# Optimization experiments

Hardware: AMD Instinct MI355X
Metric: run time of the kernel (lower is better)

The kernel has to match this reference:

```python
import jax, jax.numpy as jnp
import numpy as np

EMB = 768
HEADS = 12
DH = EMB // HEADS


def setup_inputs() -> dict:
    key = jax.random.key(0)
    k = jax.random.split(key, 5)
    s = 0.02
    return {
        "x": jax.random.normal(k[0], (4, 2048, EMB), dtype=jnp.float32),
        "qkv_w": jax.random.normal(k[1], (3 * EMB, EMB), dtype=jnp.float32) * s,  # torch Linear weight [out,in]
        "qkv_b": jax.random.normal(k[2], (3 * EMB,), dtype=jnp.float32) * s,
        "proj_w": jax.random.normal(k[3], (EMB, EMB), dtype=jnp.float32) * s,
        "proj_b": jax.random.normal(k[4], (EMB,), dtype=jnp.float32) * s,
    }


def reference(x, qkv_w, qkv_b, proj_w, proj_b):
    b, n, _ = x.shape
    qkv = x @ qkv_w.T + qkv_b  # [b, n, 3*EMB]
    # rearrange 'b n (h d qkv) -> qkv b h n d'
    qkv = qkv.reshape(b, n, HEADS, DH, 3)
    qkv = jnp.transpose(qkv, (4, 0, 2, 1, 3))  # [3, b, h, n, d]
    q, k, v = qkv[0], qkv[1], qkv[2]
    e = jnp.einsum("bhqd,bhkd->bhqk", q, k)
    scale = jnp.float32(EMB) ** 0.5
    # NOTE: original divides by sqrt(emb_size) AFTER softmax (faithful to source)
    attn = jax.nn.softmax(e, axis=-1) / scale
    out = jnp.einsum("bhqk,bhkd->bhqd", attn, v)
    out = jnp.transpose(out, (0, 2, 1, 3)).reshape(b, n, EMB)  # 'b h n d -> b n (h d)'
    return out @ proj_w.T + proj_b
```

## Files before the change

### kernel.cpp

```cpp
#include <hip/hip_runtime.h>
#include <hip/hip_bf16.h>

typedef unsigned short ushort_t;
typedef __attribute__((ext_vector_type(8))) short s16x8;
typedef __attribute__((ext_vector_type(4))) float f32x4;
typedef __attribute__((ext_vector_type(16))) float f32x16;
typedef __attribute__((ext_vector_type(4))) unsigned int u32x4;

#define EMB 768
#define HEADS 12
#define DH 64
#define BATCH 4
#define SEQ 2048
#define MTOK (BATCH*SEQ)
#define NQKV (3*EMB)
#define LOG2E 1.44269504088896f

__device__ __forceinline__ ushort_t f2bf(float f) {
  unsigned u = __float_as_uint(f);
  u += 0x7fffu + ((u >> 16) & 1u);
  return (ushort_t)(u >> 16);
}
__device__ __forceinline__ unsigned pk2bf(float a, float b) {
  return (unsigned)f2bf(a) | ((unsigned)f2bf(b) << 16);
}
__device__ __forceinline__ unsigned cvtpk(float lo, float hi_) {
  unsigned d;
  asm("v_cvt_pk_bf16_f32 %0, %1, %2" : "=v"(d) : "v"(lo), "v"(hi_));
  return d;
}

__device__ __forceinline__ void gload_lds16(const void* g, void* l) {
  __builtin_amdgcn_global_load_lds(
      (const __attribute__((address_space(1))) unsigned*)g,
      (__attribute__((address_space(3))) unsigned*)l, 16, 0, 0);
}

__global__ void cvt_bf16(const float* __restrict__ in, ushort_t* __restrict__ out, int n4) {
  int i = blockIdx.x * blockDim.x + threadIdx.x;
  if (i >= n4) return;
  const float4 v = reinterpret_cast<const float4*>(in)[i];
  reinterpret_cast<uint2*>(out)[i] = make_uint2(pk2bf(v.x, v.y), pk2bf(v.z, v.w));
}

__global__ void cvt_wqkv(const float* __restrict__ w, const float* __restrict__ bias,
                         ushort_t* __restrict__ out, float* __restrict__ bias_p, int n4) {
  int i = blockIdx.x * blockDim.x + threadIdx.x;
  if (i >= n4) return;
  const int srcrow = i / 192;
  const int c4 = i - srcrow * 192;
  const int h = srcrow / 192;
  const int rem = srcrow - h * 192;
  const int d = rem / 3;
  const int which = rem - d * 3;
  const int dstrow = which * 768 + h * 64 + d;
  const float4 v = reinterpret_cast<const float4*>(w)[i];
  reinterpret_cast<uint2*>(out)[dstrow * 192 + c4] =
      make_uint2(pk2bf(v.x, v.y), pk2bf(v.z, v.w));
  if (c4 == 0) bias_p[dstrow] = bias[srcrow];
}

#define TM 128
#define TN 128
#define NSTEP 24

template<int MODE>
__global__ __launch_bounds__(256, 3) void gemm_bt(
    const ushort_t* __restrict__ A, const ushort_t* __restrict__ BT,
    const float* __restrict__ bias, float* __restrict__ Cf,
    ushort_t* __restrict__ Qd, ushort_t* __restrict__ Kd, ushort_t* __restrict__ Vt,
    int M, int N, int K)
{
  __shared__ alignas(16) ushort_t As[3][TM*32];
  __shared__ alignas(16) ushort_t Bs[3][TN*32];
  const int t = threadIdx.x;
  const int w = t >> 6, l = t & 63, g = l >> 4, r = l & 15;
  const int wr = w >> 1, wc = w & 1;
  int lin = blockIdx.y * gridDim.x + blockIdx.x;
  const int cpx = (gridDim.x * gridDim.y) >> 3;
  lin = (lin & 7) * cpx + (lin >> 3);
  const int m0 = (lin / gridDim.x) * TM, n0 = (lin - (lin / gridDim.x) * gridDim.x) * TN;

  f32x4 acc[4][4] = {};

#define GSTAGE(bufc, st)                                                           \
  {                                                                                \
    const int kt = (st) * 32;                                                      \
    _Pragma("unroll")                                                              \
    for (int p = 0; p < 2; ++p) {                                                  \
      const int i = t + p * 256;                              \
      const int row = i >> 2, c8 = (i & 3) * 8;                                    \
      gload_lds16(A  + (size_t)(m0 + row) * K + kt + c8,                           \
                  (char*)&As[bufc][0] + i * 16);                                   \
      gload_lds16(BT + (size_t)(n0 + row) * K + kt + c8,                           \
                  (char*)&Bs[bufc][0] + i * 16);                                   \
    }                                                                              \
  }

#define GCOMP(bufc)                                                                \
  {                                                                                \
    const char* ab = (const char*)&As[bufc][0] + wr * 4096 + r * 64 + g * 16;      \
    const char* bb = (const char*)&Bs[bufc][0] + wc * 4096 + r * 64 + g * 16;      \
    s16x8 fa[4], fb[4];                                                            \
    _Pragma("unroll")                                                              \
    for (int mi = 0; mi < 4; ++mi) {                                               \
      fa[mi] = *(const s16x8*)(ab + mi * 1024);                                    \
      fb[mi] = *(const s16x8*)(bb + mi * 1024);                                    \
    }                                                                              \
    __builtin_amdgcn_s_setprio(1);                                                 \
    _Pragma("unroll")                                                              \
    for (int mi = 0; mi < 4; ++mi)                                                 \
      _Pragma("unroll")                                                            \
      for (int ni = 0; ni < 4; ++ni)                                               \
        acc[mi][ni] = __builtin_amdgcn_mfma_f32_16x16x32_bf16(                     \
            fa[mi], fb[ni], acc[mi][ni], 0, 0, 0);                                 \
    __builtin_amdgcn_s_setprio(0);                                                 \
  }

#define GITER(bufcur, bufn2, st)                                                   \
  {                                                                                \
    asm volatile("s_barrier" ::: "memory");                                        \
    { const int s2 = (st) + 2 < NSTEP ? (st) + 2 : NSTEP - 1; GSTAGE(bufn2, s2); } \
    asm volatile("s_waitcnt vmcnt(8)" ::: "memory");                               \
    asm volatile("s_barrier" ::: "memory");                                        \
    GCOMP(bufcur);                                                                 \
  }

  GSTAGE(0, 0);
  GSTAGE(1, 1);
  for (int s = 0; s < NSTEP - 3; s += 3) {
    GITER(0, 2, s);
    GITER(1, 0, s + 1);
    GITER(2, 1, s + 2);
  }
  GITER(0, 2, 21);
  GITER(1, 0, 22);
  GITER(2, 1, 23);
#undef GITER
#undef GCOMP
#undef GSTAGE

#pragma unroll
  for (int ni = 0; ni < 4; ++ni) {
    const int col = n0 + wc*64 + ni*16 + r;
    const float bv = bias[col];
    if (MODE == 0) {
#pragma unroll
      for (int mi = 0; mi < 4; ++mi)
#pragma unroll
        for (int q = 0; q < 4; ++q) {
          const int rowg = m0 + wr*64 + mi*16 + g*4 + q;
          Cf[(size_t)rowg * N + col] = acc[mi][ni][q] + bv;
        }
    } else {
      const int which = col / 768;
      const int h_ = (col - which * 768) >> 6;
      const int d_ = col & 63;
      if (which == 2) {
#pragma unroll
        for (int mi = 0; mi < 4; ++mi) {
          const int nn0 = m0 + wr*64 + mi*16 + g*4;
          const int bb = nn0 >> 11, nl = nn0 & 2047;
          const int np0 = (nl & ~12) | ((nl & 4) << 1) | ((nl & 8) >> 1);
          uint2 u;
          u.x = pk2bf(acc[mi][ni][0] + bv, acc[mi][ni][1] + bv);
          u.y = pk2bf(acc[mi][ni][2] + bv, acc[mi][ni][3] + bv);
          *reinterpret_cast<uint2*>(Vt + ((size_t)(bb*HEADS + h_)*DH + d_)*SEQ + np0) = u;
        }
      } else {
        ushort_t* dst = (which == 0) ? Qd : Kd;
        const float sc = (which == 0) ? LOG2E : 1.0f;
#pragma unroll
        for (int mi = 0; mi < 4; ++mi)
#pragma unroll
          for (int q = 0; q < 4; ++q) {
            const int rowg = m0 + wr*64 + mi*16 + g*4 + q;
            const int bb = rowg >> 11, nn = rowg & 2047;
            dst[((size_t)(bb*HEADS + h_)*SEQ + nn)*DH + d_] =
                f2bf((acc[mi][ni][q] + bv) * sc);
          }
      }
    }
  }
}

#define NTIL 32

__global__ __launch_bounds__(256, 3) void attn_fwd(
    const ushort_t* __restrict__ Qd, const ushort_t* __restrict__ Kd,
    const ushort_t* __restrict__ Vt, ushort_t* __restrict__ Oa)
{
  __shared__ alignas(16) char L[3][16384];
  char* Lc = &L[0][0];

  const int t = threadIdx.x;
  const int w = t >> 6, l = t & 63;
  const int c31 = l & 31, hi = l >> 5;
  const int blk = blockIdx.x;
  const int logical = (blk & 7) * 96 + (blk >> 3);
  const int bh = logical >> 4;
  const int qt = logical & 15;
  const int q0 = qt * 128 + w * 32;
  const int b = bh / HEADS, h = bh - b * HEADS;

  const ushort_t* Qp = Qd + (size_t)bh * SEQ * DH;
  const ushort_t* Kp = Kd + (size_t)bh * SEQ * DH;
  const ushort_t* Vp = Vt + (size_t)bh * DH * SEQ;

  s16x8 qf[4];
  {
    const ushort_t* qp = Qp + (size_t)(q0 + c31) * DH + hi * 8;
#pragma unroll
    for (int c = 0; c < 4; ++c) qf[c] = *(const s16x8*)(qp + c * 16);
  }

  f32x16 oacc0 = {}, oacc1 = {};
  float ps0 = 0.f, ps1 = 0.f, ps2 = 0.f, ps3 = 0.f;

  const int ldsb = hi * 1024 + c31 * 16;
  const ushort_t* ksrc0 = Kp + (size_t)l * DH + w * 16;
  const ushort_t* vsrc0 = Vp + (size_t)l * SEQ + w * 16;
  char* kdst0 = Lc + w * 2048 + l * 16;

#define STAGE(bufc, tile_)                                                         \
  {                                                                                \
    const int tl = (tile_);                                                        \
    const ushort_t* ks = ksrc0 + (size_t)tl * (64 * DH);                           \
    const ushort_t* vs = vsrc0 + tl * 64;                                          \
    char* kd = kdst0 + (bufc) * 16384;                                             \
    gload_lds16(ks,     kd);                                                       \
    gload_lds16(ks + 8, kd + 1024);                                                \
    gload_lds16(vs,     kd + 8192);                                                \
    gload_lds16(vs + 8, kd + 9216);                                                \
  }

#define KGROUP(bufc, kg)                                                           \
  {                                                                                \
    const char* base = Lc + (bufc) * 16384 + ldsb;                                 \
    s16x8 kf0 = *(const s16x8*)(base + ((kg)*512 + 0*2048));                       \
    s16x8 kf1 = *(const s16x8*)(base + ((kg)*512 + 1*2048));                       \
    s16x8 kf2 = *(const s16x8*)(base + ((kg)*512 + 2*2048));                       \
    s16x8 kf3 = *(const s16x8*)(base + ((kg)*512 + 3*2048));                       \
    s16x8 va00 = *(const s16x8*)(base + (8192 + (kg)*4096 + 0*2048 + 0*512));      \
    s16x8 va01 = *(const s16x8*)(base + (8192 + (kg)*4096 + 1*2048 + 0*512));      \
    s16x8 va10 = *(const s16x8*)(base + (8192 + (kg)*4096 + 0*2048 + 1*512));      \
    s16x8 va11 = *(const s16x8*)(base + (8192 + (kg)*4096 + 1*2048 + 1*512));      \
    __builtin_amdgcn_s_setprio(1);                                                 \
    f32x16 s = {};                                                                 \
    s = __builtin_amdgcn_mfma_f32_32x32x16_bf16(kf0, qf[0], s, 0, 0, 0);           \
    s = __builtin_amdgcn_mfma_f32_32x32x16_bf16(kf1, qf[1], s, 0, 0, 0);           \
    s = __builtin_amdgcn_mfma_f32_32x32x16_bf16(kf2, qf[2], s, 0, 0, 0);           \
    s = __builtin_amdgcn_mfma_f32_32x32x16_bf16(kf3, qf[3], s, 0, 0, 0);           \
    __builtin_amdgcn_s_setprio(0);                                                 \
    float pe[16];                                                                  \
    _Pragma("unroll")                                                              \
    for (int r2 = 0; r2 < 16; ++r2) pe[r2] = __builtin_amdgcn_exp2f(s[r2]);        \
    ps0 += (pe[0]  + pe[1])  + (pe[2]  + pe[3]);                                   \
    ps1 += (pe[4]  + pe[5])  + (pe[6]  + pe[7]);                                   \
    ps2 += (pe[8]  + pe[9])  + (pe[10] + pe[11]);                                  \
    ps3 += (pe[12] + pe[13]) + (pe[14] + pe[15]);                                  \
    u32x4 f0u = { cvtpk(pe[0],  pe[1]),  cvtpk(pe[2],  pe[3]),                     \
                  cvtpk(pe[4],  pe[5]),  cvtpk(pe[6],  pe[7]) };                   \
    u32x4 f1u = { cvtpk(pe[8],  pe[9]),  cvtpk(pe[10], pe[11]),                    \
                  cvtpk(pe[12], pe[13]), cvtpk(pe[14], pe[15]) };                  \
    const s16x8 pf0 = __builtin_bit_cast(s16x8, f0u);                              \
    const s16x8 pf1 = __builtin_bit_cast(s16x8, f1u);                              \
    __builtin_amdgcn_s_setprio(1);                                                 \
    oacc0 = __builtin_amdgcn_mfma_f32_32x32x16_bf16(va00, pf0, oacc0, 0, 0, 0);    \
    oacc0 = __builtin_amdgcn_mfma_f32_32x32x16_bf16(va01, pf1, oacc0, 0, 0, 0);    \
    oacc1 = __builtin_amdgcn_mfma_f32_32x32x16_bf16(va10, pf0, oacc1, 0, 0, 0);    \
    oacc1 = __builtin_amdgcn_mfma_f32_32x32x16_bf16(va11, pf1, oacc1, 0, 0, 0);    \
    __builtin_amdgcn_s_setprio(0);                                                 \
  }

#define ITER(bufcur, bufn2, tt)                                                    \
  {                                                                                \
    asm volatile("s_barrier" ::: "memory");                                        \
    const int nt2 = (tt) + 2 < NTIL ? (tt) + 2 : NTIL - 1;                         \
    STAGE(bufn2, nt2);                                                             \
    asm volatile("s_waitcnt vmcnt(8)" ::: "memory");                               \
    asm volatile("s_barrier" ::: "memory");                                        \
    KGROUP(bufcur, 0);                                                             \
    KGROUP(bufcur, 1);                                                             \
  }

  STAGE(0, 0);
  STAGE(1, 1);
  for (int tt = 0; tt < NTIL - 2; tt += 3) {
    ITER(0, 2, tt);
    ITER(1, 0, tt + 1);
    ITER(2, 1, tt + 2);
  }
  ITER(0, 2, 30);
  ITER(1, 0, 31);
#undef ITER
#undef KGROUP
#undef STAGE

  const float psum = (ps0 + ps1) + (ps2 + ps3);
  const float lt = psum + __shfl_xor(psum, 32);
  const float scale = 0.036084391824351615f / lt;

  ushort_t* op = Oa + ((size_t)(b * SEQ + q0 + c31)) * EMB + h * DH;
#pragma unroll
  for (int f = 0; f < 2; ++f) {
    const f32x16& o = f ? oacc1 : oacc0;
#pragma unroll
    for (int rq = 0; rq < 4; ++rq) {
      const int dbase = f * 32 + 8 * rq + 4 * hi;
      uint2 u;
      u.x = pk2bf(o[rq*4+0] * scale, o[rq*4+1] * scale);
      u.y = pk2bf(o[rq*4+2] * scale, o[rq*4+3] * scale);
      *reinterpret_cast<uint2*>(op + dbase) = u;
    }
  }
}

extern "C" void kernel_launch(void* const* d_in, const int* in_sizes, int n_in,
                              void* d_out, int out_size, void* d_ws, size_t ws_size,
                              hipStream_t stream) {
  const float* x      = (const float*)d_in[0];
  const float* qkv_w  = (const float*)d_in[1];
  const float* qkv_b  = (const float*)d_in[2];
  const float* proj_w = (const float*)d_in[3];
  const float* proj_b = (const float*)d_in[4];
  float* out = (float*)d_out;

  ushort_t* xb    = (ushort_t*)d_ws;
  ushort_t* wqkv  = xb    + (size_t)MTOK*EMB;
  ushort_t* wproj = wqkv  + (size_t)NQKV*EMB;
  ushort_t* Qd    = wproj + (size_t)EMB*EMB;
  ushort_t* Kd    = Qd    + (size_t)MTOK*EMB;
  ushort_t* Vt    = Kd    + (size_t)MTOK*EMB;
  ushort_t* Oa    = Vt    + (size_t)MTOK*EMB;
  float*    biasp = (float*)(Oa + (size_t)MTOK*EMB);

  {
    int n4 = MTOK*EMB/4;
    cvt_bf16<<<(n4+255)/256, 256, 0, stream>>>(x, xb, n4);
  }
  {
    int n4 = NQKV*EMB/4;
    cvt_wqkv<<<(n4+255)/256, 256, 0, stream>>>(qkv_w, qkv_b, wqkv, biasp, n4);
  }
  {
    int n4 = EMB*EMB/4;
    cvt_bf16<<<(n4+255)/256, 256, 0, stream>>>(proj_w, wproj, n4);
  }

  gemm_bt<1><<<dim3(NQKV/TN, MTOK/TM), 256, 0, stream>>>(
      xb, wqkv, biasp, nullptr, Qd, Kd, Vt, MTOK, NQKV, EMB);

  attn_fwd<<<768, 256, 0, stream>>>(Qd, Kd, Vt, Oa);

  gemm_bt<0><<<dim3(EMB/TN, MTOK/TM), 256, 0, stream>>>(
      Oa, wproj, proj_b, out, nullptr, nullptr, nullptr, MTOK, EMB, EMB);
}
```

Before: 154.0 us.

## Use BK=64 double-buffered GEMM tiles with XOR-swizzled LDS layout

The bf16 GEMM moves from three 32-wide K stages to two 64-wide K stages, which halves the number of barrier pairs per tile. The shared-memory layout gains an XOR swizzle on 128-byte rows so the wider fragment reads avoid bank conflicts. Each compute step now issues two MFMAs per accumulator. The cost is twice the LDS per stage, a launch bound lowered from 3 to 2 blocks per CU, and prefetch depth cut from two stages ahead to one.

Result: faster. 146.0 us (-5.2%).

```diff
diff --git a/kernel.cpp b/kernel.cpp
--- a/kernel.cpp
+++ b/kernel.cpp
@@ -62,17 +62,18 @@
 
 #define TM 128
 #define TN 128
-#define NSTEP 24
+#define BKG 64
+#define GSTEPS 12
 
 template<int MODE>
-__global__ __launch_bounds__(256, 3) void gemm_bt(
+__global__ __launch_bounds__(256, 2) void gemm_bt(
     const ushort_t* __restrict__ A, const ushort_t* __restrict__ BT,
     const float* __restrict__ bias, float* __restrict__ Cf,
     ushort_t* __restrict__ Qd, ushort_t* __restrict__ Kd, ushort_t* __restrict__ Vt,
     int M, int N, int K)
 {
-  __shared__ alignas(16) ushort_t As[3][TM*32];
-  __shared__ alignas(16) ushort_t Bs[3][TN*32];
+  __shared__ alignas(16) ushort_t As[2][TM*BKG];
+  __shared__ alignas(16) ushort_t Bs[2][TN*BKG];
   const int t = threadIdx.x;
   const int w = t >> 6, l = t & 63, g = l >> 4, r = l & 15;
   const int wr = w >> 1, wc = w & 1;
@@ -85,57 +86,57 @@
 
 #define GSTAGE(bufc, st)                                                           \
   {                                                                                \
-    const int kt = (st) * 32;                                                      \
+    const int kt = (st) * BKG;                                                     \
     _Pragma("unroll")                                                              \
-    for (int p = 0; p < 2; ++p) {                                                  \
-      const int i = t + p * 256;                              \
-      const int row = i >> 2, c8 = (i & 3) * 8;                                    \
-      gload_lds16(A  + (size_t)(m0 + row) * K + kt + c8,                           \
-                  (char*)&As[bufc][0] + i * 16);                                   \
-      gload_lds16(BT + (size_t)(n0 + row) * K + kt + c8,                           \
-                  (char*)&Bs[bufc][0] + i * 16);                                   \
+    for (int p = 0; p < 4; ++p) {                                                  \
+      const int off = (t + p*256) * 16;                     \
+      const int row = off >> 7;                                  \
+      const int scb = (off & 127) ^ ((row & 7) << 4);                              \
+      gload_lds16(A  + (size_t)(m0+row)*K + kt + (scb>>1), (char*)&As[bufc][0] + off); \
+      gload_lds16(BT + (size_t)(n0+row)*K + kt + (scb>>1), (char*)&Bs[bufc][0] + off); \
     }                                                                              \
   }
 
 #define GCOMP(bufc)                                                                \
   {                                                                                \
-    const char* ab = (const char*)&As[bufc][0] + wr * 4096 + r * 64 + g * 16;      \
-    const char* bb = (const char*)&Bs[bufc][0] + wc * 4096 + r * 64 + g * 16;      \
-    s16x8 fa[4], fb[4];                                                            \
+    s16x8 fa[4][2], fb[4][2];                                                      \
     _Pragma("unroll")                                                              \
-    for (int mi = 0; mi < 4; ++mi) {                                               \
-      fa[mi] = *(const s16x8*)(ab + mi * 1024);                                    \
-      fb[mi] = *(const s16x8*)(bb + mi * 1024);                                    \
-    }                                                                              \
+    for (int mi = 0; mi < 4; ++mi)                                                 \
+      _Pragma("unroll")                                                            \
+      for (int kk = 0; kk < 2; ++kk) {                                             \
+        const int ra = wr*64 + mi*16 + r;                                          \
+        fa[mi][kk] = *(const s16x8*)((const char*)&As[bufc][0] + ra*128 +          \
+                                     ((g*16 + kk*64) ^ ((ra&7)<<4)));              \
+        const int rb = wc*64 + mi*16 + r;                                          \
+        fb[mi][kk] = *(const s16x8*)((const char*)&Bs[bufc][0] + rb*128 +          \
+                                     ((g*16 + kk*64) ^ ((rb&7)<<4)));              \
+      }                                                                            \
     __builtin_amdgcn_s_setprio(1);                                                 \
     _Pragma("unroll")                                                              \
     for (int mi = 0; mi < 4; ++mi)                                                 \
       _Pragma("unroll")                                                            \
-      for (int ni = 0; ni < 4; ++ni)                                               \
+      for (int ni = 0; ni < 4; ++ni) {                                             \
         acc[mi][ni] = __builtin_amdgcn_mfma_f32_16x16x32_bf16(                     \
-            fa[mi], fb[ni], acc[mi][ni], 0, 0, 0);                                 \
+            fa[mi][0], fb[ni][0], acc[mi][ni], 0, 0, 0);                           \
+        acc[mi][ni] = __builtin_amdgcn_mfma_f32_16x16x32_bf16(                     \
+            fa[mi][1], fb[ni][1], acc[mi][ni], 0, 0, 0);                           \
+      }                                                                            \
     __builtin_amdgcn_s_setprio(0);                                                 \
   }
 
-#define GITER(bufcur, bufn2, st)                                                   \
+#define GITER(cur, st)                                                             \
   {                                                                                \
     asm volatile("s_barrier" ::: "memory");                                        \
-    { const int s2 = (st) + 2 < NSTEP ? (st) + 2 : NSTEP - 1; GSTAGE(bufn2, s2); } \
+    { const int s1 = (st) + 1 < GSTEPS ? (st) + 1 : GSTEPS - 1;                    \
+      GSTAGE((cur) ^ 1, s1); }                                                     \
     asm volatile("s_waitcnt vmcnt(8)" ::: "memory");                               \
     asm volatile("s_barrier" ::: "memory");                                        \
-    GCOMP(bufcur);                                                                 \
+    GCOMP(cur);                                                                    \
   }
 
   GSTAGE(0, 0);
-  GSTAGE(1, 1);
-  for (int s = 0; s < NSTEP - 3; s += 3) {
-    GITER(0, 2, s);
-    GITER(1, 0, s + 1);
-    GITER(2, 1, s + 2);
-  }
-  GITER(0, 2, 21);
-  GITER(1, 0, 22);
-  GITER(2, 1, 23);
+#pragma unroll
+  for (int s = 0; s < GSTEPS; ++s) GITER(s & 1, s);
 #undef GITER
 #undef GCOMP
 #undef GSTAGE
```
